# Performance work log

Measured on AMD Instinct MI355X. Metric: run time of the kernel, lower is better.

## Reference

```python
import jax, jax.numpy as jnp
import numpy as np

EPS = 1e-5       # BatchNorm2d eps
NHEAD = 8
FILL = -1e30     # stands in for scores_fill_value=-inf (finite for grad safety)


def _proj(x, w, b, g, beta, mean, var):
    # Conv2d 1x1 over NCHW (H=1) == channel matmul, followed by eval-mode BatchNorm2d.
    y = jnp.einsum('oc,bcht->boht', w, x) + b[None, :, None, None]
    inv = g * jax.lax.rsqrt(var + EPS)
    return y * inv[None, :, None, None] + (beta - mean * inv)[None, :, None, None]


def setup_inputs() -> dict:
    rng = jax.random.key(0)
    ks = jax.random.split(rng, 10)
    B, C, T = 8, 512, 1024
    query = jax.random.normal(ks[0], (B, C, 1, T), jnp.float32)
    key = jax.random.normal(ks[1], (B, C, 1, T), jnp.float32)
    value = jax.random.normal(ks[2], (B, C, 1, T), jnp.float32)
    mask = jax.random.randint(ks[3], (B, 1, T, T), 0, 2).astype(jnp.int32)
    Ws = jax.random.normal(ks[4], (4, C, C), jnp.float32) * (1.0 / np.sqrt(C))
    bs = jax.random.normal(ks[5], (4, C), jnp.float32) * 0.1
    gammas = jax.random.uniform(ks[6], (4, C), jnp.float32, 0.5, 1.5)
    betas = jax.random.normal(ks[7], (4, C), jnp.float32) * 0.1
    means = jax.random.normal(ks[8], (4, C), jnp.float32) * 0.1
    vars_ = jax.random.uniform(ks[9], (4, C), jnp.float32, 0.5, 1.5)
    return dict(query=query, key=key, value=value, mask=mask, Ws=Ws, bs=bs,
                gammas=gammas, betas=betas, means=means, vars_=vars_)


def reference(query, key, value, mask, Ws, bs, gammas, betas, means, vars_):
    B, C, _, T1 = query.shape
    T2 = key.shape[3]
    h = NHEAD
    d_k = C // h
    denom = 1.0 / np.sqrt(d_k)

    q = _proj(query, Ws[0], bs[0], gammas[0], betas[0], means[0], vars_[0]).reshape(B, h, d_k, T1)
    k = _proj(key,   Ws[1], bs[1], gammas[1], betas[1], means[1], vars_[1]).reshape(B, h, d_k, T2)
    v = _proj(value, Ws[2], bs[2], gammas[2], betas[2], means[2], vars_[2]).reshape(B, h, d_k, T2)

    # scores = k^T @ q -> (B, h, T2, T1); softmax over key axis (dim=2, matching torch)
    scores = jnp.einsum('bhds,bhdt->bhst', k, q) * denom
    mask0 = jnp.transpose(mask, (0, 1, 3, 2)) == 0  # (B, 1, T2, T1)
    scores = jnp.where(mask0, FILL, scores)
    attn = jax.nn.softmax(scores, axis=2)
    attn = jnp.where(mask0, 0.0, attn)

    # x = v @ attn -> (B, h, d_k, T1) -> (B, C, 1, T1)
    x = jnp.einsum('bhds,bhst->bhdt', v, attn).reshape(B, C, 1, T1)
    out = _proj(x, Ws[3], bs[3], gammas[3], betas[3], means[3], vars_[3])

    # cache=None branch: new_cache = cat(raw key, raw value) along channel dim
    new_cache = jnp.concatenate([key, value], axis=1)
    return (out, new_cache)
```

## Files before the change

### kernel.cpp

```cpp
#include <hip/hip_runtime.h>

typedef unsigned short u16;
typedef unsigned int   u32;
typedef short  bfrag   __attribute__((ext_vector_type(8)));
typedef float  accfrag __attribute__((ext_vector_type(16)));
typedef unsigned int   u32x4 __attribute__((ext_vector_type(4)));
typedef unsigned short u16x4 __attribute__((ext_vector_type(4)));
typedef float          f32x4 __attribute__((ext_vector_type(4)));

#define B_SZ 8
#define C_SZ 512
#define T_SZ 1024
#define NH   8
#define DK   64

#define QSCL 0.18033688f

__device__ __forceinline__ u16 f2bf(float f) {
  u32 u = __float_as_uint(f);
  u = u + 0x7fffu + ((u >> 16) & 1u);
  return (u16)(u >> 16);
}

__device__ __forceinline__ float fexp2(float x) {
  return __builtin_amdgcn_exp2f(x);
}

__device__ __forceinline__ u32 cvtpk(float lo, float hi) {
  u32 r;
  asm("v_cvt_pk_bf16_f32 %0, %1, %2" : "=v"(r) : "v"(lo), "v"(hi));
  return r;
}

__device__ __forceinline__ void permswap(u32 &a, u32 &b) {
  asm volatile("v_permlane32_swap_b32 %0, %1" : "+v"(a), "+v"(b));
}

__device__ __forceinline__ void gload16(const u16* g, u16* l) {
  __builtin_amdgcn_global_load_lds(
      (const __attribute__((address_space(1))) void*)g,
      (__attribute__((address_space(3))) void*)l, 16, 0, 0);
}

__global__ void prep_w(const float* __restrict__ Ws, const float* __restrict__ gam,
                       const float* __restrict__ var, u16* __restrict__ Wp) {
  int idx = blockIdx.x * 256 + threadIdx.x;
  int io = idx >> 9;
  float inv = gam[io] * rsqrtf(var[io] + 1e-5f);
  Wp[idx] = f2bf(Ws[idx] * inv);
}

__global__ void prep_b(const float* __restrict__ bs, const float* __restrict__ gam,
                       const float* __restrict__ beta, const float* __restrict__ mean,
                       const float* __restrict__ var, float* __restrict__ bp) {
  int idx = blockIdx.x * 256 + threadIdx.x;
  float inv = gam[idx] * rsqrtf(var[idx] + 1e-5f);
  bp[idx] = bs[idx] * inv + beta[idx] - mean[idx] * inv;
}

__global__ void transpose_cvt(const float* __restrict__ q, const float* __restrict__ k,
                              const float* __restrict__ v, u16* __restrict__ Xt,
                              float* __restrict__ cache) {
  __shared__ float tile[32][33];
  int z = blockIdx.z;
  int src = z >> 3, b = z & 7;
  const float* in = (src == 0) ? q : ((src == 1) ? k : v);
  u16* out = Xt + (size_t)src * ((size_t)B_SZ * T_SZ * C_SZ);
  int t0 = blockIdx.x * 32, c0 = blockIdx.y * 32;
  int tx = threadIdx.x & 31, ty = threadIdx.x >> 5;
#pragma unroll
  for (int rr = 0; rr < 4; ++rr) {
    int c = c0 + ty + rr * 8;
    float val = in[(((size_t)b * C_SZ + c) << 10) + t0 + tx];
    tile[ty + rr * 8][tx] = val;
    if (src >= 1) {
      int cc = c + (src == 2 ? 512 : 0);
      cache[((size_t)b << 20) + ((size_t)cc << 10) + t0 + tx] = val;
    }
  }
  __syncthreads();
#pragma unroll
  for (int rr = 0; rr < 4; ++rr) {
    int t = t0 + ty + rr * 8;
    out[(((size_t)b << 10) + t) * C_SZ + c0 + tx] = f2bf(tile[tx][ty + rr * 8]);
  }
}

__global__ void mask_bits(const int* __restrict__ mask, u32* __restrict__ mbT) {
  int w = blockIdx.x * 256 + threadIdx.x;
  int bt = w >> 5;
  int st = w & 31;
  const int* mrow = mask + ((size_t)bt << 10) + (st << 5);
  u32 word = 0;
#pragma unroll
  for (int j = 0; j < 32; j += 4) {
    int4 m4 = *(const int4*)(mrow + j);
    word |= (m4.x != 0 ? 1u : 0u) << j;
    word |= (m4.y != 0 ? 1u : 0u) << (j + 1);
    word |= (m4.z != 0 ? 1u : 0u) << (j + 2);
    word |= (m4.w != 0 ? 1u : 0u) << (j + 3);
  }
  int b = bt >> 10, t = bt & 1023;
  mbT[(((size_t)b * 32 + st) << 10) + t] = word;
}

__launch_bounds__(256, 4)
__global__ void gemm_qkv(const u16* __restrict__ Wp, const float* __restrict__ bpA,
                         const u16* __restrict__ Xt,
                         u16* __restrict__ Qf, u16* __restrict__ Kf, u16* __restrict__ Vf) {
  __shared__ __align__(16) u16 lds[2 * 128 * 64];
  int tid = threadIdx.x;
  int src = blockIdx.z >> 3;
  int b   = blockIdx.z & 7;
  int t0 = blockIdx.x * 128;
  int o0 = blockIdx.y * 128;
  int wid = tid >> 6, lane = tid & 63;
  int ln = lane & 31, hi = lane >> 5;
  int wr = wid >> 1, wc = wid & 1;

  const u16* Wsrc = Wp + (size_t)src * 262144;
  const float* bp = bpA + src * 512;
  const u16* Xin  = Xt + (size_t)src * ((size_t)B_SZ * T_SZ * C_SZ);
  u16* Yout = (src == 0) ? Qf : (src == 1 ? Kf : Vf);

  const char* Ag = (const char*)Wsrc;
  const char* Bg = (const char*)(Xin + (((size_t)b << 10) + t0) * C_SZ);
  char* ldsA = (char*)lds;
  char* ldsB = (char*)lds + 16384;

  accfrag acc[2][2];
#pragma unroll
  for (int m2 = 0; m2 < 2; ++m2)
#pragma unroll
    for (int n2 = 0; n2 < 2; ++n2)
#pragma unroll
      for (int e = 0; e < 16; ++e) acc[m2][n2][e] = 0.f;

  int lin = tid * 16;
  u32x4 ra[4], rb[4];
#pragma unroll
  for (int it = 0; it < 4; ++it) {
    int off = lin + it * 4096;
    int r = off >> 7, cb = off & 127;
    ra[it] = *(const u32x4*)(Ag + (size_t)(o0 + r) * 1024 + cb);
    rb[it] = *(const u32x4*)(Bg + (size_t)r * 1024 + cb);
  }

  for (int kt = 0; kt < 8; ++kt) {
    __syncthreads();
#pragma unroll
    for (int it = 0; it < 4; ++it) {
      int off = lin + it * 4096;
      int swz = off ^ (((off >> 7) & 7) << 4);
      *(u32x4*)(ldsA + swz) = ra[it];
      *(u32x4*)(ldsB + swz) = rb[it];
    }
    __syncthreads();
    if (kt < 7) {
#pragma unroll
      for (int it = 0; it < 4; ++it) {
        int off = lin + it * 4096;
        int r = off >> 7, cb = off & 127;
        ra[it] = *(const u32x4*)(Ag + (size_t)(o0 + r) * 1024 + (kt + 1) * 128 + cb);
        rb[it] = *(const u32x4*)(Bg + (size_t)r * 1024 + (kt + 1) * 128 + cb);
      }
    }
#pragma unroll
    for (int kk = 0; kk < 4; ++kk) {
      int csw = (kk * 32 + hi * 16) ^ ((ln & 7) << 4);
      bfrag a[2], bb[2];
#pragma unroll
      for (int m2 = 0; m2 < 2; ++m2)
        a[m2] = *(const bfrag*)(ldsA + (wr * 64 + m2 * 32 + ln) * 128 + csw);
#pragma unroll
      for (int n2 = 0; n2 < 2; ++n2)
        bb[n2] = *(const bfrag*)(ldsB + (wc * 64 + n2 * 32 + ln) * 128 + csw);
#pragma unroll
      for (int m2 = 0; m2 < 2; ++m2)
#pragma unroll
        for (int n2 = 0; n2 < 2; ++n2)
          acc[m2][n2] = __builtin_amdgcn_mfma_f32_32x32x16_bf16(a[m2], bb[n2], acc[m2][n2], 0, 0, 0);
    }
  }

  float oscl = (src == 0) ? QSCL : 1.0f;
#pragma unroll
  for (int m2 = 0; m2 < 2; ++m2) {
    int obase = o0 + wr * 64 + m2 * 32;
#pragma unroll
    for (int n2 = 0; n2 < 2; ++n2) {
      int t = t0 + wc * 64 + n2 * 32 + ln;
      if (src < 2) {
        int tt5 = t & 31, st = t >> 5;
#pragma unroll
        for (int g = 0; g < 4; ++g) {
          int d0 = obase + 8 * g + 4 * hi;
          int hh = d0 >> 6, dd = d0 & 63;
          u16x4 pk4;
#pragma unroll
          for (int qq = 0; qq < 4; ++qq)
            pk4[qq] = f2bf((acc[m2][n2][4 * g + qq] + bp[d0 + qq]) * oscl);
          size_t a = ((((size_t)b * 8 + hh) * 32 + st) << 11)
                   + (size_t)((dd >> 4) * 512 + (tt5 + 32 * ((dd >> 3) & 1)) * 8 + (dd & 7));
          *(u16x4*)(Yout + a) = pk4;
        }
      } else {
        int s = t, st = s >> 5;
#pragma unroll
        for (int r = 0; r < 16; ++r) {
          int d = obase + (r & 3) + 8 * (r >> 2) + 4 * hi;
          int hh = d >> 6, dd = d & 63;
          int fi = ((s >> 4) & 1) * 2 + ((dd >> 5) & 1);
          int l  = (dd & 31) + ((s >> 3) & 1) * 32;
          Yout[((((size_t)b * 8 + hh) * 32 + st) << 11)
               + (size_t)(fi * 512 + l * 8 + (s & 7))] = f2bf(acc[m2][n2][r] + bp[d]);
        }
      }
    }
  }
}

__launch_bounds__(256, 4)
__global__ void gemm_out(const u16* __restrict__ Wp, const float* __restrict__ bp,
                         const u16* __restrict__ Xin, float* __restrict__ Yout) {
  __shared__ __align__(16) char ldsc[24576];
  int tid = threadIdx.x;
  int b  = blockIdx.z;
  int t0 = blockIdx.x * 64;
  int o0 = blockIdx.y * 128;
  int wid = tid >> 6, lane = tid & 63;
  int ln = lane & 31, hi = lane >> 5;
  int wr = wid >> 1, wc = wid & 1;

  const char* Ag = (const char*)Wp;
  const char* Bg = (const char*)(Xin + (((size_t)b << 10) + t0) * C_SZ);
  char* ldsA = ldsc;
  char* ldsB = ldsc + 16384;

  accfrag acc[2];
#pragma unroll
  for (int m2 = 0; m2 < 2; ++m2)
#pragma unroll
    for (int e = 0; e < 16; ++e) acc[m2][e] = 0.f;

  int lin = tid * 16;
  u32x4 ra[4], rb[2];
#pragma unroll
  for (int it = 0; it < 4; ++it) {
    int off = lin + it * 4096;
    int r = off >> 7, cb = off & 127;
    ra[it] = *(const u32x4*)(Ag + (size_t)(o0 + r) * 1024 + cb);
  }
#pragma unroll
  for (int it = 0; it < 2; ++it) {
    int off = lin + it * 4096;
    int r = off >> 7, cb = off & 127;
    rb[it] = *(const u32x4*)(Bg + (size_t)r * 1024 + cb);
  }

  for (int kt = 0; kt < 8; ++kt) {
    __syncthreads();
#pragma unroll
    for (int it = 0; it < 4; ++it) {
      int off = lin + it * 4096;
      int swz = off ^ (((off >> 7) & 7) << 4);
      *(u32x4*)(ldsA + swz) = ra[it];
    }
#pragma unroll
    for (int it = 0; it < 2; ++it) {
      int off = lin + it * 4096;
      int swz = off ^ (((off >> 7) & 7) << 4);
      *(u32x4*)(ldsB + swz) = rb[it];
    }
    __syncthreads();
    if (kt < 7) {
#pragma unroll
      for (int it = 0; it < 4; ++it) {
        int off = lin + it * 4096;
        int r = off >> 7, cb = off & 127;
        ra[it] = *(const u32x4*)(Ag + (size_t)(o0 + r) * 1024 + (kt + 1) * 128 + cb);
      }
#pragma unroll
      for (int it = 0; it < 2; ++it) {
        int off = lin + it * 4096;
        int r = off >> 7, cb = off & 127;
        rb[it] = *(const u32x4*)(Bg + (size_t)r * 1024 + (kt + 1) * 128 + cb);
      }
    }
#pragma unroll
    for (int kk = 0; kk < 4; ++kk) {
      int csw = (kk * 32 + hi * 16) ^ ((ln & 7) << 4);
      bfrag a[2], bb;
#pragma unroll
      for (int m2 = 0; m2 < 2; ++m2)
        a[m2] = *(const bfrag*)(ldsA + (wr * 64 + m2 * 32 + ln) * 128 + csw);
      bb = *(const bfrag*)(ldsB + (wc * 32 + ln) * 128 + csw);
#pragma unroll
      for (int m2 = 0; m2 < 2; ++m2)
        acc[m2] = __builtin_amdgcn_mfma_f32_32x32x16_bf16(a[m2], bb, acc[m2], 0, 0, 0);
    }
  }

#pragma unroll
  for (int m2 = 0; m2 < 2; ++m2) {
    int obase = o0 + wr * 64 + m2 * 32;
    int t = t0 + wc * 32 + ln;
#pragma unroll
    for (int r = 0; r < 16; ++r) {
      int o = obase + (r & 3) + 8 * (r >> 2) + 4 * hi;
      Yout[(((size_t)b * C_SZ + o) << 10) + t] = acc[m2][r] + bp[o];
    }
  }
}

__launch_bounds__(512, 4)
__global__ void attn_fused(const u16* __restrict__ Qf, const u16* __restrict__ Kf,
                           const u16* __restrict__ Vf, const u32* __restrict__ mbT,
                           u16* __restrict__ X2) {
  __shared__ __align__(16) char smem[34816];
  float* mlb = (float*)(smem + 32768);

  int n = blockIdx.x;
  int bh = n & 63, tb = n >> 6;
  int b = bh >> 3, h = bh & 7;
  int tid = threadIdx.x;
  int wid = tid >> 6, lane = tid & 63;
  int grp = wid >> 1, wl = wid & 1;
  int ln = lane & 31, hi = lane >> 5;
  int tt = tb * 2 + wl;
  int t  = tt * 32 + ln;

  const u16* QfT = Qf + (((size_t)bh * 32 + tt) << 11);
  bfrag qf[4];
#pragma unroll
  for (int j = 0; j < 4; ++j)
    qf[j] = *(const bfrag*)(QfT + j * 512 + lane * 8);

  const u16* KfB = Kf + ((size_t)bh << 16);
  const u16* VfB = Vf + ((size_t)bh << 16);
  const u32* mcol = mbT + ((size_t)b << 15) + t;

  float m_run = -1.0e4f, l_run = 0.f;
  accfrag accd[2];
#pragma unroll
  for (int m2 = 0; m2 < 2; ++m2)
#pragma unroll
    for (int e = 0; e < 16; ++e) accd[m2][e] = 0.f;

  int gid = tid & 127;
  u16* sK = (u16*)smem + grp * 4096;
  u16* sV = sK + 2048;

  for (int it = 0; it < 8; ++it) {
    int st = grp * 8 + it;
    __syncthreads();
    {
      size_t tn = (size_t)st << 11;
      gload16(KfB + tn + gid * 8,        sK + gid * 8);
      gload16(KfB + tn + 1024 + gid * 8, sK + 1024 + gid * 8);
      gload16(VfB + tn + gid * 8,        sV + gid * 8);
      gload16(VfB + tn + 1024 + gid * 8, sV + 1024 + gid * 8);
    }
    u32 mw = mcol[st << 10];
    __syncthreads();

    bfrag kf[4], vf[4];
#pragma unroll
    for (int j = 0; j < 4; ++j) {
      kf[j] = *(const bfrag*)(sK + j * 512 + lane * 8);
      vf[j] = *(const bfrag*)(sV + j * 512 + lane * 8);
    }

    accfrag S;
#pragma unroll
    for (int e = 0; e < 16; ++e) S[e] = 0.f;
#pragma unroll
    for (int j = 0; j < 4; ++j)
      S = __builtin_amdgcn_mfma_f32_32x32x16_bf16(kf[j], qf[j], S, 0, 0, 0);

    u32 mbits = mw >> (4 * hi);
    float p[16];
#pragma unroll
    for (int r = 0; r < 16; ++r) {
      int pos = (r & 3) + 8 * (r >> 2);
      p[r] = ((mbits >> pos) & 1u) ? S[r] : -1e30f;
    }
    float q8[8], q4[4];
#pragma unroll
    for (int r = 0; r < 8; ++r) q8[r] = fmaxf(p[r], p[r + 8]);
#pragma unroll
    for (int r = 0; r < 4; ++r) q4[r] = fmaxf(q8[r], q8[r + 4]);
    float pmax = fmaxf(fmaxf(q4[0], q4[1]), fmaxf(q4[2], q4[3]));
    pmax = fmaxf(pmax, __shfl_xor(pmax, 32));

    if (__any(pmax > m_run + 11.5f)) {
      float m_new = fmaxf(m_run, pmax);
      float alpha = fexp2(m_run - m_new);
      l_run *= alpha;
#pragma unroll
      for (int m2 = 0; m2 < 2; ++m2)
#pragma unroll
        for (int e = 0; e < 16; ++e) accd[m2][e] *= alpha;
      m_run = m_new;
    }

#pragma unroll
    for (int r = 0; r < 16; ++r)
      p[r] = fexp2(p[r] - m_run);
    float s8[8], s4[4];
#pragma unroll
    for (int r = 0; r < 8; ++r) s8[r] = p[r] + p[r + 8];
#pragma unroll
    for (int r = 0; r < 4; ++r) s4[r] = s8[r] + s8[r + 4];
    float psum = (s4[0] + s4[1]) + (s4[2] + s4[3]);
    psum += __shfl_xor(psum, 32);
    l_run += psum;

    bfrag pf[2];
#pragma unroll
    for (int j2 = 0; j2 < 2; ++j2) {
      u32 A0 = cvtpk(p[8 * j2 + 0], p[8 * j2 + 1]);
      u32 A1 = cvtpk(p[8 * j2 + 2], p[8 * j2 + 3]);
      u32 B0 = cvtpk(p[8 * j2 + 4], p[8 * j2 + 5]);
      u32 B1 = cvtpk(p[8 * j2 + 6], p[8 * j2 + 7]);
      permswap(A0, B0);
      permswap(A1, B1);
      union { u32 u[4]; bfrag f; } pu;
      pu.u[0] = A0; pu.u[1] = A1; pu.u[2] = B0; pu.u[3] = B1;
      pf[j2] = pu.f;
    }
#pragma unroll
    for (int j2 = 0; j2 < 2; ++j2)
#pragma unroll
      for (int m2 = 0; m2 < 2; ++m2)
        accd[m2] = __builtin_amdgcn_mfma_f32_32x32x16_bf16(vf[j2 * 2 + m2], pf[j2], accd[m2], 0, 0, 0);
  }

  float* comb = (float*)smem;
  __syncthreads();
  if (grp & 1) {
    float* dst = comb + ((grp >> 1) * 4096 + wl * 2048);
#pragma unroll
    for (int m2 = 0; m2 < 2; ++m2)
#pragma unroll
      for (int e = 0; e < 16; ++e)
        dst[(m2 * 16 + e) * 64 + lane] = accd[m2][e];
    if (hi == 0) {
      mlb[((grp * 2 + wl) * 32 + ln) * 2]     = m_run;
      mlb[((grp * 2 + wl) * 32 + ln) * 2 + 1] = l_run;
    }
  }
  __syncthreads();
  if (!(grp & 1)) {
    int pg = grp + 1;
    const float* srcp = comb + ((pg >> 1) * 4096 + wl * 2048);
    float m1 = mlb[((pg * 2 + wl) * 32 + ln) * 2];
    float l1 = mlb[((pg * 2 + wl) * 32 + ln) * 2 + 1];
    float M  = fmaxf(m_run, m1);
    float w0 = fexp2(m_run - M), w1 = fexp2(m1 - M);
    l_run = l_run * w0 + l1 * w1;
    m_run = M;
#pragma unroll
    for (int m2 = 0; m2 < 2; ++m2)
#pragma unroll
      for (int e = 0; e < 16; ++e)
        accd[m2][e] = accd[m2][e] * w0 + srcp[(m2 * 16 + e) * 64 + lane] * w1;
  }
  __syncthreads();
  if (grp == 2) {
    float* dst = comb + wl * 2048;
#pragma unroll
    for (int m2 = 0; m2 < 2; ++m2)
#pragma unroll
      for (int e = 0; e < 16; ++e)
        dst[(m2 * 16 + e) * 64 + lane] = accd[m2][e];
    if (hi == 0) {
      mlb[((4 + wl) * 32 + ln) * 2]     = m_run;
      mlb[((4 + wl) * 32 + ln) * 2 + 1] = l_run;
    }
  }
  __syncthreads();
  if (grp == 0) {
    const float* srcp = comb + wl * 2048;
    float m1 = mlb[((4 + wl) * 32 + ln) * 2];
    float l1 = mlb[((4 + wl) * 32 + ln) * 2 + 1];
    float M  = fmaxf(m_run, m1);
    float w0 = fexp2(m_run - M), w1 = fexp2(m1 - M);
    float l  = l_run * w0 + l1 * w1;
    float invl = (l > 0.f) ? 1.f / l : 0.f;
    u16* Orow = X2 + (((size_t)b << 10) + t) * C_SZ + h * DK;
#pragma unroll
    for (int m2 = 0; m2 < 2; ++m2)
#pragma unroll
      for (int g = 0; g < 4; ++g) {
        u16x4 pk4;
#pragma unroll
        for (int qq = 0; qq < 4; ++qq) {
          int e = 4 * g + qq;
          float v2 = srcp[(m2 * 16 + e) * 64 + lane];
          pk4[qq] = f2bf((accd[m2][e] * w0 + v2 * w1) * invl);
        }
        *(u16x4*)(Orow + m2 * 32 + 8 * g + 4 * hi) = pk4;
      }
  }
}

extern "C" void kernel_launch(void* const* d_in, const int* in_sizes, int n_in,
                              void* d_out, int out_size, void* d_ws, size_t ws_size,
                              hipStream_t stream) {
  (void)in_sizes; (void)n_in; (void)out_size; (void)ws_size;
  const float* q    = (const float*)d_in[0];
  const float* k    = (const float*)d_in[1];
  const float* v    = (const float*)d_in[2];
  const int*   mask = (const int*)d_in[3];
  const float* Ws   = (const float*)d_in[4];
  const float* bs   = (const float*)d_in[5];
  const float* gam  = (const float*)d_in[6];
  const float* beta = (const float*)d_in[7];
  const float* mean = (const float*)d_in[8];
  const float* var  = (const float*)d_in[9];

  float* out   = (float*)d_out;
  float* cache = out + (size_t)B_SZ * C_SZ * T_SZ;

  const size_t ARR = (size_t)B_SZ * T_SZ * C_SZ;
  char* ws = (char*)d_ws;
  u16*   Wp = (u16*)(ws);
  float* bp = (float*)(ws + 2097152);
  u16*   Xt = (u16*)(ws + 2162688);
  u16*   Qt = Xt + 3 * ARR;
  u16*   Kt = Qt + ARR;
  u16*   Vb = Kt + ARR;
  u16*   X2 = Vb + ARR;
  u32*   mb = (u32*)((char*)(X2 + ARR));

  prep_w<<<4096, 256, 0, stream>>>(Ws, gam, var, Wp);
  prep_b<<<8, 256, 0, stream>>>(bs, gam, beta, mean, var, bp);
  transpose_cvt<<<dim3(32, 16, 24), 256, 0, stream>>>(q, k, v, Xt, cache);
  mask_bits<<<1024, 256, 0, stream>>>(mask, mb);

  gemm_qkv<<<dim3(8, 4, 24), 256, 0, stream>>>(Wp, bp, Xt, Qt, Kt, Vb);
  attn_fused<<<1024, 512, 0, stream>>>(Qt, Kt, Vb, mb, X2);
  gemm_out<<<dim3(16, 4, 8), 256, 0, stream>>>(Wp + 786432, bp + 1536, X2, out);
}
```

Before: 102.8 us.

## Prefetch next K/V tile in attention loop, raise occupancy, merge prep kernels

The attention loop now issues the LDS load for the next K/V tile and mask word right after the current fragments are read into registers, so global loads overlap the MFMA and softmax work. MFMA sections are wrapped in s_setprio raises to favour matrix issue. Launch bounds go from 4 to 8 waves-per-EU minimum, which caps registers and may cause spills. The two weight and bias prep kernels are merged into one launch to save launch overhead.

```diff
diff --git a/kernel.cpp b/kernel.cpp
--- a/kernel.cpp
+++ b/kernel.cpp
@@ -42,20 +42,21 @@
       (__attribute__((address_space(3))) void*)l, 16, 0, 0);
 }
 
-__global__ void prep_w(const float* __restrict__ Ws, const float* __restrict__ gam,
-                       const float* __restrict__ var, u16* __restrict__ Wp) {
-  int idx = blockIdx.x * 256 + threadIdx.x;
-  int io = idx >> 9;
-  float inv = gam[io] * rsqrtf(var[io] + 1e-5f);
-  Wp[idx] = f2bf(Ws[idx] * inv);
-}
-
-__global__ void prep_b(const float* __restrict__ bs, const float* __restrict__ gam,
-                       const float* __restrict__ beta, const float* __restrict__ mean,
-                       const float* __restrict__ var, float* __restrict__ bp) {
-  int idx = blockIdx.x * 256 + threadIdx.x;
-  float inv = gam[idx] * rsqrtf(var[idx] + 1e-5f);
-  bp[idx] = bs[idx] * inv + beta[idx] - mean[idx] * inv;
+__global__ void prep_wb(const float* __restrict__ Ws, const float* __restrict__ bs,
+                        const float* __restrict__ gam, const float* __restrict__ beta,
+                        const float* __restrict__ mean, const float* __restrict__ var,
+                        u16* __restrict__ Wp, float* __restrict__ bp) {
+  int bx = blockIdx.x;
+  if (bx < 4096) {
+    int idx = bx * 256 + threadIdx.x;
+    int io = idx >> 9;
+    float inv = gam[io] * rsqrtf(var[io] + 1e-5f);
+    Wp[idx] = f2bf(Ws[idx] * inv);
+  } else {
+    int idx = (bx - 4096) * 256 + threadIdx.x;
+    float inv = gam[idx] * rsqrtf(var[idx] + 1e-5f);
+    bp[idx] = bs[idx] * inv + beta[idx] - mean[idx] * inv;
+  }
 }
 
 __global__ void transpose_cvt(const float* __restrict__ q, const float* __restrict__ k,
@@ -313,7 +314,7 @@
   }
 }
 
-__launch_bounds__(512, 4)
+__launch_bounds__(512, 8)
 __global__ void attn_fused(const u16* __restrict__ Qf, const u16* __restrict__ Kf,
                            const u16* __restrict__ Vf, const u32* __restrict__ mbT,
                            u16* __restrict__ X2) {
@@ -350,33 +351,47 @@
   int gid = tid & 127;
   u16* sK = (u16*)smem + grp * 4096;
   u16* sV = sK + 2048;
+  int st0 = grp * 8;
+
+  {
+    size_t tn = (size_t)st0 << 11;
+    gload16(KfB + tn + gid * 8,        sK + gid * 8);
+    gload16(KfB + tn + 1024 + gid * 8, sK + 1024 + gid * 8);
+    gload16(VfB + tn + gid * 8,        sV + gid * 8);
+    gload16(VfB + tn + 1024 + gid * 8, sV + 1024 + gid * 8);
+  }
+  u32 mw = mcol[st0 << 10];
+  __syncthreads();
 
   for (int it = 0; it < 8; ++it) {
-    int st = grp * 8 + it;
+    int st = st0 + it;
+
+    bfrag kf[4], vf[4];
+#pragma unroll
+    for (int j = 0; j < 4; ++j) {
+      kf[j] = *(const bfrag*)(sK + j * 512 + lane * 8);
+      vf[j] = *(const bfrag*)(sV + j * 512 + lane * 8);
+    }
     __syncthreads();
-    {
-      size_t tn = (size_t)st << 11;
+
+    u32 mn = 0;
+    if (it < 7) {
+      size_t tn = (size_t)(st + 1) << 11;
       gload16(KfB + tn + gid * 8,        sK + gid * 8);
       gload16(KfB + tn + 1024 + gid * 8, sK + 1024 + gid * 8);
       gload16(VfB + tn + gid * 8,        sV + gid * 8);
       gload16(VfB + tn + 1024 + gid * 8, sV + 1024 + gid * 8);
-    }
-    u32 mw = mcol[st << 10];
-    __syncthreads();
-
-    bfrag kf[4], vf[4];
-#pragma unroll
-    for (int j = 0; j < 4; ++j) {
-      kf[j] = *(const bfrag*)(sK + j * 512 + lane * 8);
-      vf[j] = *(const bfrag*)(sV + j * 512 + lane * 8);
+      mn = mcol[(st + 1) << 10];
     }
 
     accfrag S;
 #pragma unroll
     for (int e = 0; e < 16; ++e) S[e] = 0.f;
+    __builtin_amdgcn_s_setprio(1);
 #pragma unroll
     for (int j = 0; j < 4; ++j)
       S = __builtin_amdgcn_mfma_f32_32x32x16_bf16(kf[j], qf[j], S, 0, 0, 0);
+    __builtin_amdgcn_s_setprio(0);
 
     u32 mbits = mw >> (4 * hi);
     float p[16];
@@ -429,15 +444,19 @@
       pu.u[0] = A0; pu.u[1] = A1; pu.u[2] = B0; pu.u[3] = B1;
       pf[j2] = pu.f;
     }
+    __builtin_amdgcn_s_setprio(1);
 #pragma unroll
     for (int j2 = 0; j2 < 2; ++j2)
 #pragma unroll
       for (int m2 = 0; m2 < 2; ++m2)
         accd[m2] = __builtin_amdgcn_mfma_f32_32x32x16_bf16(vf[j2 * 2 + m2], pf[j2], accd[m2], 0, 0, 0);
+    __builtin_amdgcn_s_setprio(0);
+
+    __syncthreads();
+    mw = mn;
   }
 
   float* comb = (float*)smem;
-  __syncthreads();
   if (grp & 1) {
     float* dst = comb + ((grp >> 1) * 4096 + wl * 2048);
 #pragma unroll
@@ -534,8 +553,7 @@
   u16*   X2 = Vb + ARR;
   u32*   mb = (u32*)((char*)(X2 + ARR));
 
-  prep_w<<<4096, 256, 0, stream>>>(Ws, gam, var, Wp);
-  prep_b<<<8, 256, 0, stream>>>(bs, gam, beta, mean, var, bp);
+  prep_wb<<<4104, 256, 0, stream>>>(Ws, bs, gam, beta, mean, var, Wp, bp);
   transpose_cvt<<<dim3(32, 16, 24), 256, 0, stream>>>(q, k, v, Xt, cache);
   mask_bits<<<1024, 256, 0, stream>>>(mask, mb);
 
```

After: 400.1 us. +289.2%, slower.
